# Optimization experiments

Measured on AMD Instinct MI355X. Metric: run time of the kernel, lower is better.

Reference implementation:

```python
import jax, jax.numpy as jnp
import numpy as np

N, E = 50000, 800000
IN, H, C = 256, 8, 32  # heads=8, hidden_dim=32 -> out dim 256
NEG_SLOPE = 0.2
EPS = 1e-5


def setup_inputs() -> dict:
    key = jax.random.key(0)
    ks = jax.random.split(key, 6)
    x = jax.random.normal(ks[0], (N, IN), jnp.float32)
    edge_index = jax.random.randint(ks[1], (2, E), 0, N, dtype=jnp.int32)
    W = jax.random.normal(ks[2], (IN, H * C), jnp.float32) / np.sqrt(IN).astype(np.float32)
    att_src = jax.random.normal(ks[3], (H, C), jnp.float32) * 0.1
    att_dst = jax.random.normal(ks[4], (H, C), jnp.float32) * 0.1
    bias = jnp.zeros((H * C,), jnp.float32)
    gamma = jnp.ones((H * C,), jnp.float32)
    beta = jnp.zeros((H * C,), jnp.float32)
    return {"x": x, "edge_index": edge_index, "W": W, "att_src": att_src,
            "att_dst": att_dst, "bias": bias, "gamma": gamma, "beta": beta}


def reference(x, edge_index, W, att_src, att_dst, bias, gamma, beta):
    n = x.shape[0]
    # Linear projection -> per-head features [N, H, C]
    xl = (x @ W).reshape(n, H, C)
    # Per-node attention half-logits [N, H]
    a_src = jnp.einsum('nhc,hc->nh', xl, att_src)
    a_dst = jnp.einsum('nhc,hc->nh', xl, att_dst)
    # Add self loops (PyG GATConv default)
    loops = jnp.arange(n, dtype=edge_index.dtype)
    src = jnp.concatenate([edge_index[0], loops])  # [E+N]
    dst = jnp.concatenate([edge_index[1], loops])
    # Edge attention logits + segment softmax over destination neighborhoods
    logits = jax.nn.leaky_relu(a_src[src] + a_dst[dst], NEG_SLOPE)  # [E+N, H]
    seg_max = jax.ops.segment_max(logits, dst, num_segments=n)
    ex = jnp.exp(logits - seg_max[dst])
    denom = jax.ops.segment_sum(ex, dst, num_segments=n)
    alpha = ex / denom[dst]  # [E+N, H]
    # Weighted scatter-aggregation of source features
    msgs = xl[src] * alpha[:, :, None]  # [E+N, H, C]
    out = jax.ops.segment_sum(msgs, dst, num_segments=n).reshape(n, H * C) + bias
    # LayerNorm over feature dim
    mu = jnp.mean(out, axis=-1, keepdims=True)
    var = jnp.var(out, axis=-1, keepdims=True)
    return (out - mu) / jnp.sqrt(var + EPS) * gamma + beta
```

## Files before the change

kernel.cpp:

```cpp
#include <hip/hip_runtime.h>
#include <math.h>

#define NEG 0.2f
#define LNEPS 1e-5f

typedef __attribute__((ext_vector_type(8))) short bf16x8;
typedef __attribute__((ext_vector_type(8))) unsigned short u16x8;
typedef __attribute__((ext_vector_type(4))) float f32x4;
typedef __attribute__((ext_vector_type(4))) unsigned int u32x4;

__device__ __forceinline__ float lrelu(float x){ return x > 0.f ? x : NEG*x; }

__device__ __forceinline__ short f2b(float f){
  unsigned u = __float_as_uint(f);
  unsigned r = u + 0x7fffu + ((u >> 16) & 1u);
  return (short)(r >> 16);
}
__device__ __forceinline__ float b2f(unsigned short u){
  return __uint_as_float(((unsigned)u) << 16);
}
__device__ __forceinline__ unsigned cvtpk(float lo, float hi){
  unsigned r;
  asm("v_cvt_pk_bf16_f32 %0, %1, %2" : "=v"(r) : "v"(lo), "v"(hi));
  return r;
}

__global__ __launch_bounds__(256) void wt_k(const float* __restrict__ W,
                                            const float* __restrict__ att_src,
                                            const float* __restrict__ att_dst,
                                            const int* __restrict__ dst,
                                            unsigned short* __restrict__ WT,
                                            unsigned short* __restrict__ WS,
                                            int* __restrict__ deg, int E){
  int b = blockIdx.x;
  if (b < 256){
    int idx = b*256 + threadIdx.x;
    int k = idx >> 8, c = idx & 255;
    WT[c*256 + k] = (unsigned short)f2b(W[idx]);
  } else if (b < 272){
    int idx = (b-256)*256 + threadIdx.x;
    int col = idx >> 8;
    int k   = idx & 255;
    int head = col & 7;
    const float* av = (col < 8 ? att_src : att_dst) + head*32;
    const float* wr = W + (size_t)k*256 + head*32;
    float sum = 0.f;
    #pragma unroll
    for (int c2=0;c2<32;c2++) sum += wr[c2]*av[c2];
    WS[col*256 + k] = (unsigned short)f2b(sum);
  } else {
    int e = (b-272)*256 + threadIdx.x;
    if (e < E) atomicAdd(&deg[dst[e]], 1);
  }
}

__device__ __forceinline__ void load_tile(float4 v[4], const float* __restrict__ A,
                                          int t, int M, int tid){
  const float* base = A + (size_t)t*4096;
  int rmax = M - 1 - t*16;
  #pragma unroll
  for (int j=0;j<4;j++){
    int idx4 = (j>>1)*512 + 2*tid + (j&1);
    int r = idx4 >> 6;
    if (r > rmax) idx4 = (rmax<<6) | (idx4 & 63);
    v[j] = *(const float4*)(base + (size_t)idx4*4);
  }
}

__global__ __launch_bounds__(256, 2) void mfma_gemm_k(const float* __restrict__ A,
    const unsigned short* __restrict__ WT, const unsigned short* __restrict__ WS,
    unsigned short* __restrict__ Cb,
    float* __restrict__ a_src, float* __restrict__ a_dst, int M, int nTiles){
  __shared__ __align__(16) unsigned short Asb[16*256];
  int tid = threadIdx.x;
  int w   = tid >> 6;
  int l   = tid & 63;
  int l15 = l & 15;
  int kg  = l >> 4;
  int colbase = w*64;

  bf16x8 bfr[4][8];
  #pragma unroll
  for (int j=0;j<4;j++){
    const unsigned short* bp = WT + (size_t)(colbase + j*16 + l15)*256 + kg*8;
    #pragma unroll
    for (int ks=0;ks<8;ks++) bfr[j][ks] = *(const bf16x8*)(bp + ks*32);
  }
  bf16x8 bfa[8];
  if (w==0){
    const unsigned short* bp = WS + (size_t)l15*256 + kg*8;
    #pragma unroll
    for (int ks=0;ks<8;ks++) bfa[ks] = *(const bf16x8*)(bp + ks*32);
  }

  int t = blockIdx.x;
  if (t >= nTiles) return;
  float4 v[4];
  load_tile(v, A, t, M, tid);

  while (t < nTiles){
    __syncthreads();
    #pragma unroll
    for (int p=0;p<2;p++){
      u32x4 q;
      q.x = cvtpk(v[2*p].x,   v[2*p].y);
      q.y = cvtpk(v[2*p].z,   v[2*p].w);
      q.z = cvtpk(v[2*p+1].x, v[2*p+1].y);
      q.w = cvtpk(v[2*p+1].z, v[2*p+1].w);
      int slot = p*256 + tid;
      int sw = slot ^ ((slot>>5)&7);
      *(u32x4*)(Asb + (size_t)sw*8) = q;
    }
    __syncthreads();

    int tn = t + gridDim.x;
    if (tn < nTiles) load_tile(v, A, tn, M, tid);

    f32x4 acc[4];
    #pragma unroll
    for (int j=0;j<4;j++) acc[j] = (f32x4){0.f,0.f,0.f,0.f};
    f32x4 acc_a = (f32x4){0.f,0.f,0.f,0.f};

    #pragma unroll
    for (int s=0;s<8;s++){
      int slot = l15*32 + kg + s*4;
      int sw = slot ^ (l15 & 7);
      bf16x8 af = *(const bf16x8*)(Asb + (size_t)sw*8);
      #pragma unroll
      for (int j=0;j<4;j++)
        acc[j] = __builtin_amdgcn_mfma_f32_16x16x32_bf16(af, bfr[j][s], acc[j], 0, 0, 0);
      if (w==0)
        acc_a = __builtin_amdgcn_mfma_f32_16x16x32_bf16(af, bfa[s], acc_a, 0, 0, 0);
    }

    int orow_base = t*16 + kg*4;
    #pragma unroll
    for (int j=0;j<4;j++){
      #pragma unroll
      for (int rp=0;rp<2;rp++){
        unsigned pk = cvtpk(acc[j][2*rp], acc[j][2*rp+1]);
        int orow = orow_base + 2*rp;
        if (orow < M)   Cb[(size_t)orow*256     + colbase + j*16 + l15] = (unsigned short)(pk & 0xffffu);
        if (orow+1 < M) Cb[(size_t)(orow+1)*256 + colbase + j*16 + l15] = (unsigned short)(pk >> 16);
      }
    }
    if (w==0){
      #pragma unroll
      for (int rr=0;rr<4;rr++){
        int orow = orow_base + rr;
        if (orow < M){
          if (l15 < 8) a_src[(size_t)orow*8 + l15]     = acc_a[rr];
          else         a_dst[(size_t)orow*8 + l15 - 8] = acc_a[rr];
        }
      }
    }
    t = tn;
  }
}

__global__ __launch_bounds__(1024) void scan1_k(const int* __restrict__ deg,
                                                int* __restrict__ off,
                                                int* __restrict__ bsum, int n){
  __shared__ int wsum[16];
  int tid=threadIdx.x, lane=tid&63, wid=tid>>6;
  int i = blockIdx.x*1024 + tid;
  int v = (i<n)?(deg[i]+1):0;
  int x = v;
  #pragma unroll
  for (int s=1;s<64;s<<=1){ int t2=__shfl_up(x,s); if (lane>=s) x+=t2; }
  if (lane==63) wsum[wid]=x;
  __syncthreads();
  if (tid<16){
    int y=wsum[tid];
    #pragma unroll
    for (int s=1;s<16;s<<=1){ int t2=__shfl_up(y,s); if (tid>=s) y+=t2; }
    wsum[tid]=y;
  }
  __syncthreads();
  int prefix=(wid? wsum[wid-1]:0);
  if (i<n) off[i]=prefix + x - v;
  if (tid==0) bsum[blockIdx.x]=wsum[15];
}

__global__ __launch_bounds__(1024) void scan3self_k(int* __restrict__ off,
    const int* __restrict__ bsum, int* __restrict__ sorted, int* __restrict__ cur,
    int n, int total){
  __shared__ int prefs;
  if (threadIdx.x < 64){
    int v = ((int)threadIdx.x < blockIdx.x) ? bsum[threadIdx.x] : 0;
    #pragma unroll
    for (int s=1;s<64;s<<=1) v += __shfl_xor(v, s);
    if (threadIdx.x==0) prefs = v;
  }
  __syncthreads();
  int i = blockIdx.x*1024 + threadIdx.x;
  if (blockIdx.x==0 && threadIdx.x==0) off[n] = total;
  if (i>=n) return;
  int o = off[i] + prefs;
  off[i] = o;
  sorted[o] = i;
  cur[i] = 1;
}

__global__ void scatter_k(const int* __restrict__ src, const int* __restrict__ dst,
                          const int* __restrict__ off, int* __restrict__ cur,
                          int* __restrict__ sorted, int E){
  int e=blockIdx.x*blockDim.x+threadIdx.x;
  if (e<E){
    int d=dst[e];
    int pos=off[d]+atomicAdd(&cur[d],1);
    sorted[pos]=src[e];
  }
}

__global__ __launch_bounds__(256) void agg5_k(const unsigned short* __restrict__ xlb,
    const float* __restrict__ a_src, const float* __restrict__ a_dst,
    const int* __restrict__ off, const int* __restrict__ sorted,
    const float* __restrict__ bias, const float* __restrict__ gamma,
    const float* __restrict__ beta, float* __restrict__ out, int n){
  int node = blockIdx.x*4 + (threadIdx.x>>6);
  if (node >= n) return;
  int lane = threadIdx.x & 63;
  int half = lane >> 5;
  int sl   = lane & 31;
  int h    = sl >> 2;
  int hh   = lane & 7;
  int je   = lane >> 3;
  float adst_h = a_dst[(size_t)node*8 + h];
  float adst_e = a_dst[(size_t)node*8 + hh];
  int s0 = off[node], dd = off[node+1] - s0;

  float acc[8] = {0.f,0.f,0.f,0.f,0.f,0.f,0.f,0.f};
  float den = 0.f;

  int i = 0;
  for (; i+8 <= dd; i += 8){
    int s[4];
    #pragma unroll
    for (int j=0;j<4;j++) s[j] = sorted[s0 + i + 2*j + half];
    int se = sorted[s0 + i + je];
    float w_l = __expf(lrelu(a_src[(size_t)se*8 + hh] + adst_e));
    float wv[4];
    #pragma unroll
    for (int j=0;j<4;j++) wv[j] = __shfl(w_l, ((2*j+half)<<3) | h);
    u16x8 u[4];
    #pragma unroll
    for (int j=0;j<4;j++) u[j] = *(const u16x8*)(xlb + (size_t)s[j]*256 + sl*8);
    #pragma unroll
    for (int j=0;j<4;j++){
      den += wv[j];
      #pragma unroll
      for (int k=0;k<8;k++) acc[k] += wv[j]*b2f((unsigned short)u[j][k]);
    }
  }
  for (; i < dd; i += 2){
    int idx = i + half;
    bool ok = idx < dd;
    int s1 = ok ? sorted[s0+idx] : node;
    float w1 = ok ? __expf(lrelu(a_src[(size_t)s1*8+h]+adst_h)) : 0.f;
    u16x8 u1 = *(const u16x8*)(xlb + (size_t)s1*256 + sl*8);
    den += w1;
    #pragma unroll
    for (int k=0;k<8;k++) acc[k] += w1*b2f((unsigned short)u1[k]);
  }

  den += __shfl_xor(den, 32);
  #pragma unroll
  for (int k=0;k<8;k++) acc[k] += __shfl_xor(acc[k], 32);

  float rd = 1.0f/den;
  float4 bia0 = *(const float4*)(bias + sl*8);
  float4 bia1 = *(const float4*)(bias + sl*8 + 4);
  float o[8];
  o[0]=acc[0]*rd+bia0.x; o[1]=acc[1]*rd+bia0.y; o[2]=acc[2]*rd+bia0.z; o[3]=acc[3]*rd+bia0.w;
  o[4]=acc[4]*rd+bia1.x; o[5]=acc[5]*rd+bia1.y; o[6]=acc[6]*rd+bia1.z; o[7]=acc[7]*rd+bia1.w;

  float sum=0.f, ssq=0.f;
  #pragma unroll
  for (int k=0;k<8;k++){ sum += o[k]; ssq += o[k]*o[k]; }
  #pragma unroll
  for (int s=1;s<32;s<<=1){ sum += __shfl_xor(sum,s); ssq += __shfl_xor(ssq,s); }
  float mean = sum*(1.0f/256.0f);
  float var  = ssq*(1.0f/256.0f) - mean*mean;
  float rstd = rsqrtf(var + LNEPS);

  int f = sl*8 + half*4;
  float4 g  = *(const float4*)(gamma + f);
  float4 be = *(const float4*)(beta + f);
  int kb = half*4;
  float4 ov;
  ov.x = (o[kb+0]-mean)*rstd*g.x+be.x;
  ov.y = (o[kb+1]-mean)*rstd*g.y+be.y;
  ov.z = (o[kb+2]-mean)*rstd*g.z+be.z;
  ov.w = (o[kb+3]-mean)*rstd*g.w+be.w;
  *(float4*)(out + (size_t)node*256 + f) = ov;
}

extern "C" void kernel_launch(void* const* d_in, const int* in_sizes, int n_in,
                              void* d_out, int out_size, void* d_ws, size_t ws_size,
                              hipStream_t stream){
  const float* x       = (const float*)d_in[0];
  const int*   ei      = (const int*)  d_in[1];
  const float* W       = (const float*)d_in[2];
  const float* att_src = (const float*)d_in[3];
  const float* att_dst = (const float*)d_in[4];
  const float* bias    = (const float*)d_in[5];
  const float* gamma   = (const float*)d_in[6];
  const float* beta    = (const float*)d_in[7];
  float* out = (float*)d_out;

  int N = in_sizes[0]/256;
  int E = in_sizes[1]/2;
  const int* srcp = ei;
  const int* dstp = ei + E;

  unsigned short* xlb = (unsigned short*)d_ws;
  float* a_src = (float*)(xlb + (size_t)N*256);
  float* a_dst = a_src + (size_t)N*8;
  int*   deg   = (int*)(a_dst + (size_t)N*8);
  int*   off   = deg + N;
  int*   cur   = off + N + 1;
  int*   sorted= cur + N;
  int*   bsum  = sorted + E + N;
  unsigned short* WT = (unsigned short*)(bsum + 1024);
  unsigned short* WS = WT + 65536;

  int nb = (N + 1023)/1024;
  int nTiles = (N + 15)/16;

  hipMemsetAsync(deg, 0, (size_t)N*sizeof(int), stream);
  wt_k<<<272 + (E+255)/256, 256, 0, stream>>>(W, att_src, att_dst, dstp, WT, WS, deg, E);
  mfma_gemm_k<<<512, 256, 0, stream>>>(x, WT, WS, xlb, a_src, a_dst, N, nTiles);
  scan1_k<<<nb, 1024, 0, stream>>>(deg, off, bsum, N);
  scan3self_k<<<nb, 1024, 0, stream>>>(off, bsum, sorted, cur, N, E + N);
  scatter_k<<<(E+255)/256, 256, 0, stream>>>(srcp, dstp, off, cur, sorted, E);
  agg5_k<<<(N+3)/4, 256, 0, stream>>>(xlb, a_src, a_dst, off, sorted, bias, gamma, beta, out, N);
}
```

Before: 193.9 us.

## Fuse CSR edge scatter into GEMM kernel and vectorize transposed output stores

The edge scatter now runs as extra blocks of the GEMM kernel, and the scans move ahead of the GEMM so both workloads share one launch and can overlap. The MFMA operands are swapped so each lane holds four consecutive columns of one row. This allows packed 8-byte bf16 stores and float4 stores of the attention logits, which are now interleaved into a single src/dst array. The aim is to remove a launch and the serialization between GEMM and scatter, and to replace scattered 2-byte stores with coalesced wide ones. The cost is that scatter blocks compete with GEMM blocks for CUs, and the scans no longer overlap the GEMM.

```diff
diff --git a/kernel.cpp b/kernel.cpp
--- a/kernel.cpp
+++ b/kernel.cpp
@@ -3,6 +3,7 @@
 
 #define NEG 0.2f
 #define LNEPS 1e-5f
+#define GB 512
 
 typedef __attribute__((ext_vector_type(8))) short bf16x8;
 typedef __attribute__((ext_vector_type(8))) unsigned short u16x8;
@@ -54,6 +55,50 @@
   }
 }
 
+__global__ __launch_bounds__(1024) void scan1_k(const int* __restrict__ deg,
+                                                int* __restrict__ off,
+                                                int* __restrict__ bsum, int n){
+  __shared__ int wsum[16];
+  int tid=threadIdx.x, lane=tid&63, wid=tid>>6;
+  int i = blockIdx.x*1024 + tid;
+  int v = (i<n)?(deg[i]+1):0;
+  int x = v;
+  #pragma unroll
+  for (int s=1;s<64;s<<=1){ int t2=__shfl_up(x,s); if (lane>=s) x+=t2; }
+  if (lane==63) wsum[wid]=x;
+  __syncthreads();
+  if (tid<16){
+    int y=wsum[tid];
+    #pragma unroll
+    for (int s=1;s<16;s<<=1){ int t2=__shfl_up(y,s); if (tid>=s) y+=t2; }
+    wsum[tid]=y;
+  }
+  __syncthreads();
+  int prefix=(wid? wsum[wid-1]:0);
+  if (i<n) off[i]=prefix + x - v;
+  if (tid==0) bsum[blockIdx.x]=wsum[15];
+}
+
+__global__ __launch_bounds__(1024) void scan3self_k(int* __restrict__ off,
+    const int* __restrict__ bsum, int* __restrict__ sorted, int* __restrict__ cur,
+    int n, int total){
+  __shared__ int prefs;
+  if (threadIdx.x < 64){
+    int v = ((int)threadIdx.x < blockIdx.x) ? bsum[threadIdx.x] : 0;
+    #pragma unroll
+    for (int s=1;s<64;s<<=1) v += __shfl_xor(v, s);
+    if (threadIdx.x==0) prefs = v;
+  }
+  __syncthreads();
+  int i = blockIdx.x*1024 + threadIdx.x;
+  if (blockIdx.x==0 && threadIdx.x==0) off[n] = total;
+  if (i>=n) return;
+  int o = off[i] + prefs;
+  off[i] = o;
+  sorted[o] = i;
+  cur[i] = 1;
+}
+
 __device__ __forceinline__ void load_tile(float4 v[4], const float* __restrict__ A,
                                           int t, int M, int tid){
   const float* base = A + (size_t)t*4096;
@@ -67,12 +112,25 @@
   }
 }
 
-__global__ __launch_bounds__(256, 2) void mfma_gemm_k(const float* __restrict__ A,
+__global__ __launch_bounds__(256, 2) void gemm_scat_k(const float* __restrict__ A,
     const unsigned short* __restrict__ WT, const unsigned short* __restrict__ WS,
-    unsigned short* __restrict__ Cb,
-    float* __restrict__ a_src, float* __restrict__ a_dst, int M, int nTiles){
+    unsigned short* __restrict__ Cb, float* __restrict__ asd, int M, int nTiles,
+    const int* __restrict__ src, const int* __restrict__ dst,
+    const int* __restrict__ off, int* __restrict__ cur,
+    int* __restrict__ sorted, int E){
   __shared__ __align__(16) unsigned short Asb[16*256];
   int tid = threadIdx.x;
+
+  if (blockIdx.x >= GB){
+    int e = (blockIdx.x - GB)*256 + tid;
+    if (e < E){
+      int d = dst[e];
+      int pos = off[d] + atomicAdd(&cur[d], 1);
+      sorted[pos] = src[e];
+    }
+    return;
+  }
+
   int w   = tid >> 6;
   int l   = tid & 63;
   int l15 = l & 15;
@@ -113,7 +171,7 @@
     }
     __syncthreads();
 
-    int tn = t + gridDim.x;
+    int tn = t + GB;
     if (tn < nTiles) load_tile(v, A, tn, M, tid);
 
     f32x4 acc[4];
@@ -128,93 +186,32 @@
       bf16x8 af = *(const bf16x8*)(Asb + (size_t)sw*8);
       #pragma unroll
       for (int j=0;j<4;j++)
-        acc[j] = __builtin_amdgcn_mfma_f32_16x16x32_bf16(af, bfr[j][s], acc[j], 0, 0, 0);
+        acc[j] = __builtin_amdgcn_mfma_f32_16x16x32_bf16(bfr[j][s], af, acc[j], 0, 0, 0);
       if (w==0)
-        acc_a = __builtin_amdgcn_mfma_f32_16x16x32_bf16(af, bfa[s], acc_a, 0, 0, 0);
-    }
-
-    int orow_base = t*16 + kg*4;
-    #pragma unroll
-    for (int j=0;j<4;j++){
+        acc_a = __builtin_amdgcn_mfma_f32_16x16x32_bf16(bfa[s], af, acc_a, 0, 0, 0);
+    }
+
+    int row = t*16 + l15;
+    if (row < M){
+      unsigned short* cp = Cb + (size_t)row*256 + colbase + kg*4;
       #pragma unroll
-      for (int rp=0;rp<2;rp++){
-        unsigned pk = cvtpk(acc[j][2*rp], acc[j][2*rp+1]);
-        int orow = orow_base + 2*rp;
-        if (orow < M)   Cb[(size_t)orow*256     + colbase + j*16 + l15] = (unsigned short)(pk & 0xffffu);
-        if (orow+1 < M) Cb[(size_t)(orow+1)*256 + colbase + j*16 + l15] = (unsigned short)(pk >> 16);
+      for (int j=0;j<4;j++){
+        uint2 pk;
+        pk.x = cvtpk(acc[j][0], acc[j][1]);
+        pk.y = cvtpk(acc[j][2], acc[j][3]);
+        *(uint2*)(cp + j*16) = pk;
       }
-    }
-    if (w==0){
-      #pragma unroll
-      for (int rr=0;rr<4;rr++){
-        int orow = orow_base + rr;
-        if (orow < M){
-          if (l15 < 8) a_src[(size_t)orow*8 + l15]     = acc_a[rr];
-          else         a_dst[(size_t)orow*8 + l15 - 8] = acc_a[rr];
-        }
+      if (w==0){
+        float4 av = {acc_a[0], acc_a[1], acc_a[2], acc_a[3]};
+        *(float4*)(asd + (size_t)row*16 + kg*4) = av;
       }
     }
     t = tn;
   }
 }
 
-__global__ __launch_bounds__(1024) void scan1_k(const int* __restrict__ deg,
-                                                int* __restrict__ off,
-                                                int* __restrict__ bsum, int n){
-  __shared__ int wsum[16];
-  int tid=threadIdx.x, lane=tid&63, wid=tid>>6;
-  int i = blockIdx.x*1024 + tid;
-  int v = (i<n)?(deg[i]+1):0;
-  int x = v;
-  #pragma unroll
-  for (int s=1;s<64;s<<=1){ int t2=__shfl_up(x,s); if (lane>=s) x+=t2; }
-  if (lane==63) wsum[wid]=x;
-  __syncthreads();
-  if (tid<16){
-    int y=wsum[tid];
-    #pragma unroll
-    for (int s=1;s<16;s<<=1){ int t2=__shfl_up(y,s); if (tid>=s) y+=t2; }
-    wsum[tid]=y;
-  }
-  __syncthreads();
-  int prefix=(wid? wsum[wid-1]:0);
-  if (i<n) off[i]=prefix + x - v;
-  if (tid==0) bsum[blockIdx.x]=wsum[15];
-}
-
-__global__ __launch_bounds__(1024) void scan3self_k(int* __restrict__ off,
-    const int* __restrict__ bsum, int* __restrict__ sorted, int* __restrict__ cur,
-    int n, int total){
-  __shared__ int prefs;
-  if (threadIdx.x < 64){
-    int v = ((int)threadIdx.x < blockIdx.x) ? bsum[threadIdx.x] : 0;
-    #pragma unroll
-    for (int s=1;s<64;s<<=1) v += __shfl_xor(v, s);
-    if (threadIdx.x==0) prefs = v;
-  }
-  __syncthreads();
-  int i = blockIdx.x*1024 + threadIdx.x;
-  if (blockIdx.x==0 && threadIdx.x==0) off[n] = total;
-  if (i>=n) return;
-  int o = off[i] + prefs;
-  off[i] = o;
-  sorted[o] = i;
-  cur[i] = 1;
-}
-
-__global__ void scatter_k(const int* __restrict__ src, const int* __restrict__ dst,
-                          const int* __restrict__ off, int* __restrict__ cur,
-                          int* __restrict__ sorted, int E){
-  int e=blockIdx.x*blockDim.x+threadIdx.x;
-  if (e<E){
-    int d=dst[e];
-    int pos=off[d]+atomicAdd(&cur[d],1);
-    sorted[pos]=src[e];
-  }
-}
-
 __global__ __launch_bounds__(256) void agg5_k(const unsigned short* __restrict__ xlb,
-    const float* __restrict__ a_src, const float* __restrict__ a_dst,
+    const float* __restrict__ asd,
     const int* __restrict__ off, const int* __restrict__ sorted,
     const float* __restrict__ bias, const float* __restrict__ gamma,
     const float* __restrict__ beta, float* __restrict__ out, int n){
@@ -226,8 +223,8 @@
   int h    = sl >> 2;
   int hh   = lane & 7;
   int je   = lane >> 3;
-  float adst_h = a_dst[(size_t)node*8 + h];
-  float adst_e = a_dst[(size_t)node*8 + hh];
+  float adst_h = asd[(size_t)node*16 + 8 + h];
+  float adst_e = asd[(size_t)node*16 + 8 + hh];
   int s0 = off[node], dd = off[node+1] - s0;
 
   float acc[8] = {0.f,0.f,0.f,0.f,0.f,0.f,0.f,0.f};
@@ -239,7 +236,7 @@
     #pragma unroll
     for (int j=0;j<4;j++) s[j] = sorted[s0 + i + 2*j + half];
     int se = sorted[s0 + i + je];
-    float w_l = __expf(lrelu(a_src[(size_t)se*8 + hh] + adst_e));
+    float w_l = __expf(lrelu(asd[(size_t)se*16 + hh] + adst_e));
     float wv[4];
     #pragma unroll
     for (int j=0;j<4;j++) wv[j] = __shfl(w_l, ((2*j+half)<<3) | h);
@@ -257,7 +254,7 @@
     int idx = i + half;
     bool ok = idx < dd;
     int s1 = ok ? sorted[s0+idx] : node;
-    float w1 = ok ? __expf(lrelu(a_src[(size_t)s1*8+h]+adst_h)) : 0.f;
+    float w1 = ok ? __expf(lrelu(asd[(size_t)s1*16 + h] + adst_h)) : 0.f;
     u16x8 u1 = *(const u16x8*)(xlb + (size_t)s1*256 + sl*8);
     den += w1;
     #pragma unroll
@@ -315,9 +312,8 @@
   const int* dstp = ei + E;
 
   unsigned short* xlb = (unsigned short*)d_ws;
-  float* a_src = (float*)(xlb + (size_t)N*256);
-  float* a_dst = a_src + (size_t)N*8;
-  int*   deg   = (int*)(a_dst + (size_t)N*8);
+  float* asd   = (float*)(xlb + (size_t)N*256);
+  int*   deg   = (int*)(asd + (size_t)N*16);
   int*   off   = deg + N;
   int*   cur   = off + N + 1;
   int*   sorted= cur + N;
@@ -327,12 +323,13 @@
 
   int nb = (N + 1023)/1024;
   int nTiles = (N + 15)/16;
+  int scatBlocks = (E + 255)/256;
 
   hipMemsetAsync(deg, 0, (size_t)N*sizeof(int), stream);
-  wt_k<<<272 + (E+255)/256, 256, 0, stream>>>(W, att_src, att_dst, dstp, WT, WS, deg, E);
-  mfma_gemm_k<<<512, 256, 0, stream>>>(x, WT, WS, xlb, a_src, a_dst, N, nTiles);
+  wt_k<<<272 + scatBlocks, 256, 0, stream>>>(W, att_src, att_dst, dstp, WT, WS, deg, E);
   scan1_k<<<nb, 1024, 0, stream>>>(deg, off, bsum, N);
   scan3self_k<<<nb, 1024, 0, stream>>>(off, bsum, sorted, cur, N, E + N);
-  scatter_k<<<(E+255)/256, 256, 0, stream>>>(srcp, dstp, off, cur, sorted, E);
-  agg5_k<<<(N+3)/4, 256, 0, stream>>>(xlb, a_src, a_dst, off, sorted, bias, gamma, beta, out, N);
-}
+  gemm_scat_k<<<GB + scatBlocks, 256, 0, stream>>>(x, WT, WS, xlb, asd, N, nTiles,
+                                                   srcp, dstp, off, cur, sorted, E);
+  agg5_k<<<(N+3)/4, 256, 0, stream>>>(xlb, asd, off, sorted, bias, gamma, beta, out, N);
+}
```

New measurement: 183.9 us. 1.05x faster.
